# Kernel tuning notes

Measured on AMD Instinct MI355X. Metric: run time of the kernel, lower is better.

The kernel has to match this reference:

```python
import jax, jax.numpy as jnp
import numpy as np
from jax import lax

RADIUS = 0.3
NSAMPLE = 16
NPROP = 256
NHB = 12
NSC = 18
NCLS = 18
BNEPS = 1e-5


def setup_inputs() -> dict:
    key = jax.random.key(0)
    ks = jax.random.split(key, 10)
    B, K, C = 32, 2048, 256
    OUT = 2 + 3 + NHB * 2 + NSC * 4 + NCLS  # 119
    return {
        "xyz": jax.random.uniform(ks[0], (B, K, 3), jnp.float32),
        "features": jax.random.normal(ks[1], (B, C, K), jnp.float32),
        "sa_w1": jax.random.normal(ks[2], (256, C + 3), jnp.float32) * 0.05,
        "sa_w2": jax.random.normal(ks[3], (256, 256), jnp.float32) * 0.05,
        "sa_w3": jax.random.normal(ks[4], (256, 256), jnp.float32) * 0.05,
        "sa_gamma": jnp.ones((3, 256), jnp.float32),
        "sa_beta": jnp.zeros((3, 256), jnp.float32),
        "sa_mean": jnp.zeros((3, 256), jnp.float32),
        "sa_var": jnp.ones((3, 256), jnp.float32),
        "p_w1": jax.random.normal(ks[5], (256, 256), jnp.float32) * 0.05,
        "p_w2": jax.random.normal(ks[6], (256, 256), jnp.float32) * 0.05,
        "p_w3": jax.random.normal(ks[7], (OUT, 256), jnp.float32) * 0.05,
        "p_b3": jnp.zeros((OUT,), jnp.float32),
        "p_gamma": jnp.ones((2, 256), jnp.float32),
        "p_beta": jnp.zeros((2, 256), jnp.float32),
        "p_mean": jnp.zeros((2, 256), jnp.float32),
        "p_var": jnp.ones((2, 256), jnp.float32),
        "mean_size_arr": jax.random.uniform(ks[8], (NSC, 3), jnp.float32, 0.3, 1.5),
    }


def fps(xyz, npoint):
    # iterative furthest point sampling, starts at index 0 (matches CUDA kernel)
    B, K, _ = xyz.shape

    def body(carry, _):
        dist, far = carry
        centroid = jnp.take_along_axis(xyz, far[:, None, None], axis=1)  # (B,1,3)
        d = jnp.sum((xyz - centroid) ** 2, axis=-1)  # (B,K)
        dist = jnp.minimum(dist, d)
        nxt = jnp.argmax(dist, axis=-1).astype(jnp.int32)
        return (dist, nxt), far

    init = (jnp.full((B, K), 1e10, xyz.dtype), jnp.zeros((B,), jnp.int32))
    _, inds = lax.scan(body, init, None, length=npoint)
    return jnp.transpose(inds, (1, 0))  # (B, npoint)


def ball_query(new_xyz, xyz):
    # first NSAMPLE points (in original index order) within RADIUS; pad with first hit
    B, K, _ = xyz.shape
    d2 = jnp.sum((new_xyz[:, :, None, :] - xyz[:, None, :, :]) ** 2, axis=-1)  # (B,P,K)
    within = d2 < RADIUS * RADIUS
    cand = jnp.where(within, jnp.arange(K, dtype=jnp.int32)[None, None, :], K)
    cand = jnp.sort(cand, axis=-1)[..., :NSAMPLE]
    first = cand[..., :1]  # query point itself is always within radius
    return jnp.where(cand == K, first, cand)  # (B,P,NSAMPLE)


def box_corners(center_unnorm, size, angle):
    # flip_axis_to_camera: X right, Y down (-z_up), Z forward (y_up)
    cc = jnp.stack([center_unnorm[..., 0], center_unnorm[..., 2], -center_unnorm[..., 1]], axis=-1)
    c, s = jnp.cos(angle), jnp.sin(angle)
    zz, oo = jnp.zeros_like(angle), jnp.ones_like(angle)
    R = jnp.stack([c, zz, s, zz, oo, zz, -s, zz, c], axis=-1).reshape(angle.shape + (3, 3))
    sx = jnp.asarray([1, 1, -1, -1, 1, 1, -1, -1], jnp.float32)
    sy = jnp.asarray([1, 1, 1, 1, -1, -1, -1, -1], jnp.float32)
    sz = jnp.asarray([1, -1, -1, 1, 1, -1, -1, 1], jnp.float32)
    xc = size[..., 0:1] * sx * 0.5
    yc = size[..., 2:3] * sy * 0.5
    zc = size[..., 1:2] * sz * 0.5
    corners = jnp.stack([xc, yc, zc], axis=-2)  # (B,P,3,8)
    out = jnp.einsum('bpij,bpjk->bpik', R, corners) + cc[..., None]
    return jnp.transpose(out, (0, 1, 3, 2))  # (B,P,8,3)


def _forward(xyz, features, sa_w1, sa_w2, sa_w3, sa_gamma, sa_beta, sa_mean, sa_var,
             p_w1, p_w2, p_w3, p_b3, p_gamma, p_beta, p_mean, p_var, mean_size_arr):
    B, K, _ = xyz.shape
    inds = fps(xyz, NPROP)  # (B,P) vote_fps
    new_xyz = jnp.take_along_axis(xyz, inds[..., None], axis=1)  # (B,P,3)
    idx = ball_query(new_xyz, xyz)  # (B,P,S)
    flat = idx.reshape(B, -1)
    g_xyz = jnp.take_along_axis(xyz, flat[..., None], axis=1).reshape(B, NPROP, NSAMPLE, 3)
    g_xyz = (g_xyz - new_xyz[:, :, None, :]) / RADIUS  # normalize_xyz
    g_feat = jnp.take_along_axis(features, flat[:, None, :], axis=2).reshape(B, -1, NPROP, NSAMPLE)
    x = jnp.concatenate([jnp.transpose(g_xyz, (0, 3, 1, 2)), g_feat], axis=1)  # (B,3+C,P,S)
    for i, w in enumerate((sa_w1, sa_w2, sa_w3)):
        x = jnp.einsum('oc,bcps->bops', w, x)
        scale = (sa_gamma[i] / jnp.sqrt(sa_var[i] + BNEPS))[None, :, None, None]
        x = jax.nn.relu((x - sa_mean[i][None, :, None, None]) * scale + sa_beta[i][None, :, None, None])
    y = jnp.max(x, axis=-1)  # (B,256,P) max-pool over neighbors
    for i, w in enumerate((p_w1, p_w2)):
        y = jnp.einsum('oc,bcp->bop', w, y)
        scale = (p_gamma[i] / jnp.sqrt(p_var[i] + BNEPS))[None, :, None]
        y = jax.nn.relu((y - p_mean[i][None, :, None]) * scale + p_beta[i][None, :, None])
    net = jnp.einsum('oc,bcp->bop', p_w3, y) + p_b3[None, :, None]
    nt = jnp.transpose(net, (0, 2, 1))  # (B,P,119)
    obj = nt[..., 0:2]
    center = new_xyz + nt[..., 2:5]
    o = 5 + NHB * 2
    size_scores = nt[..., o:o + NSC]
    srn = nt[..., o + NSC:o + NSC * 4].reshape(B, NPROP, NSC, 3)
    sem = nt[..., o + NSC * 4:]
    size_res = srn * mean_size_arr[None, None]
    best = jnp.argmax(size_scores, axis=-1)
    pred_size = jnp.take_along_axis(size_res + mean_size_arr[None, None],
                                    best[..., None, None], axis=2)[:, :, 0, :]
    corners = box_corners(center, pred_size, jnp.zeros_like(center[..., 0]))
    sem_logits = jnp.concatenate(
        [sem, jnp.argmin(obj, axis=-1, keepdims=True).astype(nt.dtype) * 1e10], axis=-1)
    obj_prob = jax.nn.softmax(obj, axis=-1)[..., 1]
    sem_prob = jax.nn.softmax(sem, axis=-1)
    return obj, center, size_scores, size_res, pred_size, sem, corners, sem_logits, obj_prob, sem_prob


def reference(xyz, features, sa_w1, sa_w2, sa_w3, sa_gamma, sa_beta, sa_mean, sa_var,
              p_w1, p_w2, p_w3, p_b3, p_gamma, p_beta, p_mean, p_var, mean_size_arr):
    return _forward(xyz, features, sa_w1, sa_w2, sa_w3, sa_gamma, sa_beta, sa_mean, sa_var,
                    p_w1, p_w2, p_w3, p_b3, p_gamma, p_beta, p_mean, p_var, mean_size_arr)
```

## Files before the change

### kernel.cpp

```cpp
#include <hip/hip_runtime.h>
#include <math.h>

#define B_   32
#define K_   2048
#define C_   256
#define P_   256
#define S_   16
#define OUTC 119

#define OFF0 0
#define OFF1 16384
#define OFF2 40960
#define OFF3 188416
#define OFF4 630784
#define OFF5 655360
#define OFF6 802816
#define OFF7 999424
#define OFF8 1155072
#define OFF9 1163264

typedef _Float16 half8  __attribute__((ext_vector_type(8)));
typedef _Float16 half4h __attribute__((ext_vector_type(4)));
typedef float    f32x4  __attribute__((ext_vector_type(4)));
#define MFMA16 __builtin_amdgcn_mfma_f32_16x16x32_f16

__device__ __forceinline__ float sqdist_rn(float ax, float ay, float az,
                                           float bx, float by, float bz) {
  float dx = __fsub_rn(ax, bx), dy = __fsub_rn(ay, by), dz = __fsub_rn(az, bz);
  return __fadd_rn(__fadd_rn(__fmul_rn(dx, dx), __fmul_rn(dy, dy)),
                   __fmul_rn(dz, dz));
}

__device__ __forceinline__ unsigned umax_(unsigned a, unsigned b) {
  return a > b ? a : b;
}
__device__ __forceinline__ unsigned umin_(unsigned a, unsigned b) {
  return a < b ? a : b;
}
__device__ __forceinline__ unsigned wave_red_umax(unsigned x) {
  x = umax_(x, (unsigned)__builtin_amdgcn_update_dpp(0, (int)x, 0x111, 0xf, 0xf, false));
  x = umax_(x, (unsigned)__builtin_amdgcn_update_dpp(0, (int)x, 0x112, 0xf, 0xf, false));
  x = umax_(x, (unsigned)__builtin_amdgcn_update_dpp(0, (int)x, 0x114, 0xf, 0xf, false));
  x = umax_(x, (unsigned)__builtin_amdgcn_update_dpp(0, (int)x, 0x118, 0xf, 0xf, false));
  x = umax_(x, (unsigned)__builtin_amdgcn_update_dpp(0, (int)x, 0x142, 0xf, 0xf, false));
  x = umax_(x, (unsigned)__builtin_amdgcn_update_dpp(0, (int)x, 0x143, 0xf, 0xf, false));
  return x;
}
__device__ __forceinline__ unsigned wave_red_umin(unsigned x) {
  x = umin_(x, (unsigned)__builtin_amdgcn_update_dpp(-1, (int)x, 0x111, 0xf, 0xf, false));
  x = umin_(x, (unsigned)__builtin_amdgcn_update_dpp(-1, (int)x, 0x112, 0xf, 0xf, false));
  x = umin_(x, (unsigned)__builtin_amdgcn_update_dpp(-1, (int)x, 0x114, 0xf, 0xf, false));
  x = umin_(x, (unsigned)__builtin_amdgcn_update_dpp(-1, (int)x, 0x118, 0xf, 0xf, false));
  x = umin_(x, (unsigned)__builtin_amdgcn_update_dpp(-1, (int)x, 0x142, 0xf, 0xf, false));
  x = umin_(x, (unsigned)__builtin_amdgcn_update_dpp(-1, (int)x, 0x143, 0xf, 0xf, false));
  return x;
}

__device__ __forceinline__ void wsplit_body(
    int r, int t, const float* __restrict__ w1, const float* __restrict__ w2,
    const float* __restrict__ w3, const float* __restrict__ pw1,
    const float* __restrict__ pw2, const float* __restrict__ gma,
    const float* __restrict__ var, const float* __restrict__ pg,
    const float* __restrict__ pv, _Float16* __restrict__ w1h,
    _Float16* __restrict__ w1l, _Float16* __restrict__ w2h,
    _Float16* __restrict__ w2l, _Float16* __restrict__ w3h,
    _Float16* __restrict__ w3l, _Float16* __restrict__ p1h,
    _Float16* __restrict__ p1l, _Float16* __restrict__ p2h,
    _Float16* __restrict__ p2l, float* __restrict__ bns) {
  if (r == 656) {
    for (int u = t; u < 768; u += 64) bns[u] = gma[u] / sqrtf(var[u] + 1e-5f);
    for (int u = t; u < 512; u += 64)
      bns[768 + u] = pg[u] / sqrtf(pv[u] + 1e-5f);
    return;
  }
  const float* src;
  _Float16 *dh, *dl;
  int ot, ks, nks, K, remap = 0;
  if (r < 144) {
    src = w1; dh = w1h; dl = w1l; ot = r / 9; ks = r % 9; nks = 9; K = 259;
    remap = 1;
  } else if (r < 272) {
    const int rr = r - 144;
    src = w2; dh = w2h; dl = w2l; ot = rr >> 3; ks = rr & 7; nks = 8; K = 256;
  } else if (r < 400) {
    const int rr = r - 272;
    src = w3; dh = w3h; dl = w3l; ot = rr >> 3; ks = rr & 7; nks = 8; K = 256;
  } else if (r < 528) {
    const int rr = r - 400;
    src = pw1; dh = p1h; dl = p1l; ot = rr >> 3; ks = rr & 7; nks = 8; K = 256;
  } else {
    const int rr = r - 528;
    src = pw2; dh = p2h; dl = p2l; ot = rr >> 3; ks = rr & 7; nks = 8; K = 256;
  }
  const int m = t & 15, q = t >> 4;
  const float* row = src + (ot * 16 + m) * K;
  half8 vh, vl;
#pragma unroll
  for (int j = 0; j < 8; j++) {
    const int c = ks * 32 + q * 8 + j;
    float v;
    if (remap) {
      v = (c < 3) ? row[c] : (c >= 8 && c < 264) ? row[c - 5] : 0.f;
    } else {
      v = (c < K) ? row[c] : 0.f;
    }
    const _Float16 hi = (_Float16)v;
    vh[j] = hi;
    vl[j] = (_Float16)(v - (float)hi);
  }
  const int base = ((ot * nks + ks) * 64 + t) * 8;
  *(half8*)&dh[base] = vh;
  *(half8*)&dl[base] = vl;
}

__global__ __launch_bounds__(256) void fused_pre_kernel(
    const float* __restrict__ xyz, float* __restrict__ new_xyz,
    const float* __restrict__ features, _Float16* __restrict__ ftH,
    _Float16* __restrict__ ftL,
    const float* __restrict__ w1, const float* __restrict__ w2,
    const float* __restrict__ w3, const float* __restrict__ pw1,
    const float* __restrict__ pw2, const float* __restrict__ gma,
    const float* __restrict__ var, const float* __restrict__ pg,
    const float* __restrict__ pv, _Float16* __restrict__ w1h,
    _Float16* __restrict__ w1l, _Float16* __restrict__ w2h,
    _Float16* __restrict__ w2l, _Float16* __restrict__ w3h,
    _Float16* __restrict__ w3l, _Float16* __restrict__ p1h,
    _Float16* __restrict__ p1l, _Float16* __restrict__ p2h,
    _Float16* __restrict__ p2l, float* __restrict__ bns) {
  __shared__ __align__(16) char smem_pre[32768];
  __shared__ uint2 redw[2][4];
  const int bid = blockIdx.x;

  if (bid >= 197) {
    const int idx = bid - 197;
    const int b = idx >> 7, rem = idx & 127;
    const int c0 = (rem >> 5) * 64, k0 = (rem & 31) * 64;
    float* tl = (float*)smem_pre;
    const int w = threadIdx.x >> 6, lane = threadIdx.x & 63;
    const float* fb = features + (size_t)b * C_ * K_;
#pragma unroll
    for (int r = 0; r < 16; r++) {
      const int cl = r * 4 + w;
      tl[cl * 65 + lane] = fb[(size_t)(c0 + cl) * K_ + k0 + lane];
    }
    __syncthreads();
#pragma unroll
    for (int r = 0; r < 16; r++) {
      const int kl = r * 4 + w;
      const float v = tl[lane * 65 + kl];
      const _Float16 hi = (_Float16)v;
      const size_t o = ((size_t)b * K_ + k0 + kl) * C_ + c0 + lane;
      ftH[o] = hi;
      ftL[o] = (_Float16)(v - (float)hi);
    }
    return;
  }

  if (bid >= 32) {
    const int sub = (bid - 32) * 4 + (threadIdx.x >> 6);
    if (sub < 657)
      wsplit_body(sub, threadIdx.x & 63, w1, w2, w3, pw1, pw2, gma, var, pg,
                  pv, w1h, w1l, w2h, w2l, w3h, w3l, p1h, p1l, p2h, p2l, bns);
    return;
  }

  const int b = bid, t = threadIdx.x;
  const int lane = t & 63, w = t >> 6;
  float4* pts = (float4*)smem_pre;
  const float* xb = xyz + b * K_ * 3;
  float px[8], py[8], pz[8], dist[8];
#pragma unroll
  for (int j = 0; j < 8; j++) {
    const int k = t + 256 * j;
    const float x = xb[3 * k + 0];
    const float yv = xb[3 * k + 1];
    const float z = xb[3 * k + 2];
    px[j] = x; py[j] = yv; pz[j] = z;
    dist[j] = 1e10f;
    pts[k] = make_float4(x, yv, z, 0.f);
  }
  __syncthreads();
  int far = 0;
  for (int i = 0; i < P_; i++) {
    const float4 c = pts[far];
    if (t == 0) {
      float* nx = new_xyz + (b * P_ + i) * 3;
      nx[0] = c.x; nx[1] = c.y; nx[2] = c.z;
    }
    float bv = -1.f;
    int bj = 0;
#pragma unroll
    for (int j = 0; j < 8; j++) {
      const float d = sqdist_rn(px[j], py[j], pz[j], c.x, c.y, c.z);
      dist[j] = fminf(dist[j], d);
      if (dist[j] > bv) { bv = dist[j]; bj = j; }
    }
    const unsigned bvb = __float_as_uint(bv);
    const unsigned gw = wave_red_umax(bvb);
    const unsigned gmaxw = (unsigned)__builtin_amdgcn_readlane((int)gw, 63);
    const unsigned kg = (unsigned)(bj * 256 + t);
    const unsigned key2 = (bvb == gmaxw) ? kg : 0xFFFFFFFFu;
    const unsigned kw = wave_red_umin(key2);
    if (lane == 63) redw[i & 1][w] = make_uint2(gmaxw, kw);
    __syncthreads();
    const uint2 r0 = redw[i & 1][0], r1 = redw[i & 1][1];
    const uint2 r2 = redw[i & 1][2], r3 = redw[i & 1][3];
    const unsigned g = umax_(umax_(r0.x, r1.x), umax_(r2.x, r3.x));
    unsigned fk = 0xFFFFFFFFu;
    if (r0.x == g) fk = umin_(fk, r0.y);
    if (r1.x == g) fk = umin_(fk, r1.y);
    if (r2.x == g) fk = umin_(fk, r2.y);
    if (r3.x == g) fk = umin_(fk, r3.y);
    far = (int)fk;
  }
}

__global__ __launch_bounds__(1024) void ballq_kernel(
    const float* __restrict__ xyz, const float* __restrict__ new_xyz,
    int* __restrict__ idxw) {
  const int blk = blockIdx.x;
  const int b = blk >> 4, pg = (blk & 15) * 16, t = threadIdx.x;
  __shared__ __align__(16) float4 pts[K_];
  const float* xb = xyz + b * K_ * 3;
#pragma unroll
  for (int j = 0; j < 2; j++) {
    const int k = t + 1024 * j;
    pts[k] = make_float4(xb[3 * k + 0], xb[3 * k + 1], xb[3 * k + 2], 0.f);
  }
  __syncthreads();
  const float r2 = (float)(0.3 * 0.3);
  const int w = t >> 6, lane = t & 63;
  const int p = pg + w;
  const float nx = new_xyz[(b * P_ + p) * 3 + 0];
  const float ny = new_xyz[(b * P_ + p) * 3 + 1];
  const float nz = new_xyz[(b * P_ + p) * 3 + 2];
  int* ob = idxw + (b * P_ + p) * S_;
  unsigned msk = 0u;
#pragma unroll
  for (int j = 0; j < 32; j++) {
    const float4 q = pts[j * 64 + lane];
    const float d2 = sqdist_rn(q.x, q.y, q.z, nx, ny, nz);
    msk |= (d2 < r2 ? 1u : 0u) << j;
  }
  int cnt = 0, first = -1;
  for (int j = 0; j < 32; j++) {
    const unsigned long long bal = __ballot((msk >> j) & 1u);
    if (bal != 0ull && first < 0) first = j * 64 + (__ffsll(bal) - 1);
    const int c = (int)__popcll(bal);
    if ((msk >> j) & 1u) {
      const int pos = cnt + (int)__popcll(bal & ((1ull << lane) - 1ull));
      if (pos < S_) ob[pos] = j * 64 + lane;
    }
    cnt += c;
    if (cnt >= S_) break;
  }
  if (cnt < S_ && lane < S_ - cnt) ob[cnt + lane] = first;
}

__global__ __launch_bounds__(512, 4) void sa_kernel(
    const float* __restrict__ xyz, const float* __restrict__ features,
    const _Float16* __restrict__ ftH, const _Float16* __restrict__ ftL,
    const int use_ft,
    const _Float16* __restrict__ w1h, const _Float16* __restrict__ w1l,
    const _Float16* __restrict__ w2h, const _Float16* __restrict__ w2l,
    const _Float16* __restrict__ w3h, const _Float16* __restrict__ w3l,
    const float* __restrict__ bns, const float* __restrict__ mu,
    const float* __restrict__ bta, const float* __restrict__ new_xyz,
    const int* __restrict__ idxw, float* __restrict__ y) {
  const int blk = blockIdx.x;
  const int b = blk >> 7, p0 = (blk & 127) * 2, t = threadIdx.x;
  __shared__ __align__(16) _Float16 X1h[18 * 64 * 8];
  __shared__ __align__(16) _Float16 X1l[18 * 64 * 8];
  __shared__ __align__(16) _Float16 X2h[16 * 64 * 8];
  __shared__ __align__(16) _Float16 X2l[16 * 64 * 8];
  __shared__ __align__(16) float red[2 * 256];
  __shared__ int k_sh[32];

  if (t < 32) k_sh[t] = idxw[(b * P_ + p0) * S_ + t];
  if (t < 96) {
    const int tile = 16 + (t / 48), rem = t % 48;
    const int row = tile * 64 + 16 + rem;
    const half8 z8 = {};
    *(half8*)&X1h[row * 8] = z8;
    *(half8*)&X1l[row * 8] = z8;
  }
  __syncthreads();
  if (t < 32) {
    const int st = t >> 4, m = t & 15, k = k_sh[t];
    const float* xb = xyz + b * K_ * 3;
    const float* nx = new_xyz + (b * P_ + p0 + st) * 3;
    const int base = (st * 64 + m) * 8;
#pragma unroll
    for (int c = 0; c < 3; c++) {
      const float v = (xb[3 * k + c] - nx[c]) / 0.3f;
      const _Float16 hi = (_Float16)v;
      X1h[base + c] = hi;
      X1l[base + c] = (_Float16)(v - (float)hi);
    }
#pragma unroll
    for (int j = 3; j < 8; j++) {
      X1h[base + j] = (_Float16)0.f;
      X1l[base + j] = (_Float16)0.f;
    }
  }
  if (use_ft) {
    for (int u = t; u < 1024; u += 512) {
      const int s = u >> 5, ch = u & 31;
      const int c = 8 + ch * 8;
      const int ks = c >> 5, q2 = (c >> 3) & 3;
      const int st = s >> 4, m = s & 15;
      const size_t ro = ((size_t)b * K_ + k_sh[s]) * C_ + ch * 8;
      const int dst = ((ks * 2 + st) * 64 + q2 * 16 + m) * 8;
      *(half8*)&X1h[dst] = *(const half8*)&ftH[ro];
      *(half8*)&X1l[dst] = *(const half8*)&ftL[ro];
    }
  } else {
    const int cl = t & 255, hf = t >> 8;
    const float* fb = features + (size_t)b * C_ * K_ + (size_t)cl * K_;
    const int c = 8 + cl;
    const int ks = c >> 5, q2 = (c >> 3) & 3, j = c & 7;
    const int s0 = hf * 16;
#pragma unroll 8
    for (int s = s0; s < s0 + 16; s++) {
      const float v = fb[k_sh[s]];
      const _Float16 hi = (_Float16)v;
      const int dst = ((ks * 2 + (s >> 4)) * 64 + q2 * 16 + (s & 15)) * 8 + j;
      X1h[dst] = hi;
      X1l[dst] = (_Float16)(v - (float)hi);
    }
  }

  const int lane = t & 63, w = t >> 6;
  const int m = lane & 15, q = lane >> 4;

  f32x4 acc[2][2];
  half8 rAh[2][2], rAl[2][2];
#pragma unroll
  for (int i = 0; i < 2; i++) {
    rAh[0][i] = *(const half8*)&w1h[(((2 * w + i) * 9 + 0) * 64 + lane) * 8];
    rAl[0][i] = *(const half8*)&w1l[(((2 * w + i) * 9 + 0) * 64 + lane) * 8];
    rAh[1][i] = *(const half8*)&w1h[(((2 * w + i) * 9 + 1) * 64 + lane) * 8];
    rAl[1][i] = *(const half8*)&w1l[(((2 * w + i) * 9 + 1) * 64 + lane) * 8];
  }
  __syncthreads();

#pragma unroll
  for (int l = 0; l < 3; l++) {
    const _Float16* Xih = (l == 1) ? X2h : X1h;
    const _Float16* Xil = (l == 1) ? X2l : X1l;
    const int nks = (l == 0) ? 9 : 8;
    const int base = (l == 0) ? 0 : (l == 1) ? 9 : 17;
#pragma unroll
    for (int i = 0; i < 2; i++) {
      acc[i][0] = (f32x4){0.f, 0.f, 0.f, 0.f};
      acc[i][1] = (f32x4){0.f, 0.f, 0.f, 0.f};
    }
#pragma unroll
    for (int ks = 0; ks < nks; ks++) {
      const int par = (base + ks) & 1;
      half8 Ah[2], Al[2];
#pragma unroll
      for (int i = 0; i < 2; i++) { Ah[i] = rAh[par][i]; Al[i] = rAl[par][i]; }
      {
        int ln = l, kn = ks + 2;
        if (kn >= nks) { kn -= nks; ln = l + 1; }
        if (ln < 3) {
          const _Float16* Ph = (ln == 0) ? w1h : (ln == 1) ? w2h : w3h;
          const _Float16* Pl = (ln == 0) ? w1l : (ln == 1) ? w2l : w3l;
          const int nk2 = (ln == 0) ? 9 : 8;
#pragma unroll
          for (int i = 0; i < 2; i++) {
            const int off = (((2 * w + i) * nk2 + kn) * 64 + lane) * 8;
            rAh[par][i] = *(const half8*)&Ph[off];
            rAl[par][i] = *(const half8*)&Pl[off];
          }
        }
      }
      const int tb = (ks * 2) * 512 + lane * 8;
      const half8 Bh0 = *(const half8*)&Xih[tb];
      const half8 Bl0 = *(const half8*)&Xil[tb];
      const half8 Bh1 = *(const half8*)&Xih[tb + 512];
      const half8 Bl1 = *(const half8*)&Xil[tb + 512];
#pragma unroll
      for (int i = 0; i < 2; i++) {
        acc[i][0] = MFMA16(Ah[i], Bh0, acc[i][0], 0, 0, 0);
        acc[i][0] = MFMA16(Ah[i], Bl0, acc[i][0], 0, 0, 0);
        acc[i][0] = MFMA16(Al[i], Bh0, acc[i][0], 0, 0, 0);
        acc[i][1] = MFMA16(Ah[i], Bh1, acc[i][1], 0, 0, 0);
        acc[i][1] = MFMA16(Ah[i], Bl1, acc[i][1], 0, 0, 0);
        acc[i][1] = MFMA16(Al[i], Bh1, acc[i][1], 0, 0, 0);
      }
    }

    if (l < 2) {
      _Float16* Xoh = (l == 0) ? X2h : X1h;
      _Float16* Xol = (l == 0) ? X2l : X1l;
#pragma unroll
      for (int i = 0; i < 2; i++) {
        const int c0 = (2 * w + i) * 16 + q * 4;
        const int ks2 = c0 >> 5, q2 = (c0 >> 3) & 3, j0 = c0 & 7;
        const f32x4 sc4 = *(const f32x4*)&bns[l * 256 + c0];
        const f32x4 m4 = *(const f32x4*)&mu[l * 256 + c0];
        const f32x4 b4 = *(const f32x4*)&bta[l * 256 + c0];
#pragma unroll
        for (int s = 0; s < 2; s++) {
          half4h vh, vl;
#pragma unroll
          for (int r = 0; r < 4; r++) {
            const float v = fmaxf((acc[i][s][r] - m4[r]) * sc4[r] + b4[r], 0.f);
            const _Float16 hi = (_Float16)v;
            vh[r] = hi;
            vl[r] = (_Float16)(v - (float)hi);
          }
          const int dst = ((ks2 * 2 + s) * 64 + q2 * 16 + m) * 8 + j0;
          *(half4h*)&Xoh[dst] = vh;
          *(half4h*)&Xol[dst] = vl;
        }
      }
      __syncthreads();
    } else {
#pragma unroll
      for (int i = 0; i < 2; i++)
#pragma unroll
        for (int s = 0; s < 2; s++)
#pragma unroll
          for (int r = 0; r < 4; r++) {
            float v = acc[i][s][r];
            v = fmaxf(v, __shfl_xor(v, 1));
            v = fmaxf(v, __shfl_xor(v, 2));
            v = fmaxf(v, __shfl_xor(v, 4));
            v = fmaxf(v, __shfl_xor(v, 8));
            acc[i][s][r] = v;
          }
      if (m == 0) {
#pragma unroll
        for (int i = 0; i < 2; i++) {
          const int ob = (2 * w + i) * 16 + q * 4;
          *(f32x4*)&red[ob] = acc[i][0];
          *(f32x4*)&red[256 + ob] = acc[i][1];
        }
      }
      __syncthreads();
      const int pl = t >> 8, col = t & 255;
      const float sc2 = bns[512 + col];
      const float mu2 = mu[512 + col], bt2 = bta[512 + col];
      const float raw = red[pl * 256 + col];
      y[(b * P_ + p0 + pl) * 256 + col] = fmaxf((raw - mu2) * sc2 + bt2, 0.f);
    }
  }
}

__global__ __launch_bounds__(256, 2) void phead_kernel(
    const float* __restrict__ y, const _Float16* __restrict__ p1h,
    const _Float16* __restrict__ p1l, const _Float16* __restrict__ p2h,
    const _Float16* __restrict__ p2l, const float* __restrict__ pw3,
    const float* __restrict__ pb3, const float* __restrict__ bns,
    const float* __restrict__ pm, const float* __restrict__ pb,
    const float* __restrict__ new_xyz, const float* __restrict__ msa,
    float* __restrict__ out) {
  const int blk = blockIdx.x;
  const int b = blk >> 4, p0 = (blk & 15) * 16, t = threadIdx.x;
  __shared__ __align__(16) char smem[58624];
  _Float16* X0h = (_Float16*)smem;
  _Float16* X0l = (_Float16*)(smem + 8448);
  _Float16* Hh  = (_Float16*)(smem + 16896);
  _Float16* Hl  = (_Float16*)(smem + 25344);
  float*    Wt  = (float*)smem;
  float*    Y2  = (float*)(smem + 33792);
  float*    net_s = (float*)(smem + 50432);

  {
#pragma unroll 4
    for (int s = 0; s < 16; s++) {
      const float v = y[(size_t)(b * P_ + p0 + s) * C_ + t];
      const _Float16 hi = (_Float16)v;
      X0h[s * 264 + t] = hi;
      X0l[s * 264 + t] = (_Float16)(v - (float)hi);
    }
  }
  const int lane = t & 63, w = t >> 6;
  const int m = lane & 15, q = lane >> 4;

  f32x4 acc[4];
  half8 pAh[4], pAl[4];
#pragma unroll
  for (int i = 0; i < 4; i++) {
    const int off = (((4 * w + i) * 8) * 64 + lane) * 8;
    pAh[i] = *(const half8*)&p1h[off];
    pAl[i] = *(const half8*)&p1l[off];
  }
  __syncthreads();

#pragma unroll
  for (int l = 0; l < 2; l++) {
    const _Float16* Xih = l ? Hh : X0h;
    const _Float16* Xil = l ? Hl : X0l;
#pragma unroll
    for (int i = 0; i < 4; i++) acc[i] = (f32x4){0.f, 0.f, 0.f, 0.f};
    for (int ks = 0; ks < 8; ks++) {
      half8 Ah[4], Al[4];
#pragma unroll
      for (int i = 0; i < 4; i++) { Ah[i] = pAh[i]; Al[i] = pAl[i]; }
      {
        int ln = l, kn = ks + 1;
        if (kn == 8) { ln = l + 1; kn = 0; }
        if (ln < 2) {
          const _Float16* Ph = ln ? p2h : p1h;
          const _Float16* Pl = ln ? p2l : p1l;
#pragma unroll
          for (int i = 0; i < 4; i++) {
            const int off = (((4 * w + i) * 8 + kn) * 64 + lane) * 8;
            pAh[i] = *(const half8*)&Ph[off];
            pAl[i] = *(const half8*)&Pl[off];
          }
        }
      }
      const int xo = ks * 32 + q * 8;
      const half8 Bh = *(const half8*)&Xih[m * 264 + xo];
      const half8 Bl = *(const half8*)&Xil[m * 264 + xo];
#pragma unroll
      for (int i = 0; i < 4; i++) {
        acc[i] = MFMA16(Ah[i], Bh, acc[i], 0, 0, 0);
        acc[i] = MFMA16(Ah[i], Bl, acc[i], 0, 0, 0);
        acc[i] = MFMA16(Al[i], Bh, acc[i], 0, 0, 0);
      }
    }
#pragma unroll
    for (int i = 0; i < 4; i++) {
      const int ob = (4 * w + i) * 16 + q * 4;
      const f32x4 sc4 = *(const f32x4*)&bns[768 + l * 256 + ob];
      const f32x4 m4 = *(const f32x4*)&pm[l * 256 + ob];
      const f32x4 b4 = *(const f32x4*)&pb[l * 256 + ob];
      if (l == 0) {
        half4h vh, vl;
#pragma unroll
        for (int r = 0; r < 4; r++) {
          const float v = fmaxf((acc[i][r] - m4[r]) * sc4[r] + b4[r], 0.f);
          const _Float16 hi = (_Float16)v;
          vh[r] = hi;
          vl[r] = (_Float16)(v - (float)hi);
        }
        *(half4h*)&Hh[m * 264 + ob] = vh;
        *(half4h*)&Hl[m * 264 + ob] = vl;
      } else {
        f32x4 r4;
#pragma unroll
        for (int r = 0; r < 4; r++)
          r4[r] = fmaxf((acc[i][r] - m4[r]) * sc4[r] + b4[r], 0.f);
        *(f32x4*)&Y2[m * 260 + ob] = r4;
      }
    }
    __syncthreads();
  }

  {
    const int o = t & 127, ph = t >> 7;
    float a3[8];
#pragma unroll
    for (int pp = 0; pp < 8; pp++) a3[pp] = 0.f;
    for (int tile = 0; tile < 16; tile++) {
      const int c0 = tile * 16;
      for (int u = t; u < 119 * 4; u += 256) {
        int oo = u >> 2, qq = u & 3;
        *(float4*)&Wt[(qq * 128 + oo) * 4] =
            *(const float4*)(pw3 + oo * 256 + c0 + qq * 4);
      }
      __syncthreads();
      if (o < 119) {
#pragma unroll
        for (int j4 = 0; j4 < 4; j4++) {
          const float4 wv = *(const float4*)&Wt[(j4 * 128 + o) * 4];
#pragma unroll
          for (int pp = 0; pp < 8; pp++) {
            const float4 xv =
                *(const float4*)&Y2[(ph * 8 + pp) * 260 + c0 + j4 * 4];
            a3[pp] = fmaf(wv.x, xv.x, a3[pp]);
            a3[pp] = fmaf(wv.y, xv.y, a3[pp]);
            a3[pp] = fmaf(wv.z, xv.z, a3[pp]);
            a3[pp] = fmaf(wv.w, xv.w, a3[pp]);
          }
        }
      }
      __syncthreads();
    }
    if (o < 119) {
      const float bb = pb3[o];
#pragma unroll
      for (int pp = 0; pp < 8; pp++)
        net_s[(ph * 8 + pp) * 120 + o] = a3[pp] + bb;
    }
  }
  __syncthreads();

  if (t < 16) {
    const int gi = b * P_ + p0 + t;
    const float* nr = &net_s[t * 120];
    const float nx = new_xyz[gi * 3 + 0];
    const float ny = new_xyz[gi * 3 + 1];
    const float nz = new_xyz[gi * 3 + 2];
    const float obj0 = nr[0], obj1 = nr[1];
    out[OFF0 + gi * 2 + 0] = obj0;
    out[OFF0 + gi * 2 + 1] = obj1;
    const float cx = nx + nr[2], cy = ny + nr[3], cz = nz + nr[4];
    out[OFF1 + gi * 3 + 0] = cx;
    out[OFF1 + gi * 3 + 1] = cy;
    out[OFF1 + gi * 3 + 2] = cz;
    float bv = -1e30f;
    int bi = 0;
#pragma unroll
    for (int i = 0; i < 18; i++) {
      float v = nr[29 + i];
      out[OFF2 + gi * 18 + i] = v;
      if (v > bv) { bv = v; bi = i; }
    }
#pragma unroll
    for (int i = 0; i < 18; i++)
#pragma unroll
      for (int j = 0; j < 3; j++)
        out[OFF3 + gi * 54 + i * 3 + j] =
            __fmul_rn(nr[47 + i * 3 + j], msa[i * 3 + j]);
    float ps[3];
#pragma unroll
    for (int j = 0; j < 3; j++) {
      ps[j] = __fadd_rn(__fmul_rn(nr[47 + bi * 3 + j], msa[bi * 3 + j]),
                        msa[bi * 3 + j]);
      out[OFF4 + gi * 3 + j] = ps[j];
    }
    float sm = -1e30f;
#pragma unroll
    for (int i = 0; i < 18; i++) {
      float v = nr[101 + i];
      out[OFF5 + gi * 18 + i] = v;
      out[OFF7 + gi * 19 + i] = v;
      sm = fmaxf(sm, v);
    }
    out[OFF7 + gi * 19 + 18] = (obj0 <= obj1) ? 0.f : 1e10f;
    const float cc0 = cx, cc1 = cz, cc2 = -cy;
    const float sxk[8] = {1, 1, -1, -1, 1, 1, -1, -1};
    const float syk[8] = {1, 1, 1, 1, -1, -1, -1, -1};
    const float szk[8] = {1, -1, -1, 1, 1, -1, -1, 1};
#pragma unroll
    for (int k = 0; k < 8; k++) {
      out[OFF6 + gi * 24 + 3 * k + 0] = cc0 + ps[0] * sxk[k] * 0.5f;
      out[OFF6 + gi * 24 + 3 * k + 1] = cc1 + ps[2] * syk[k] * 0.5f;
      out[OFF6 + gi * 24 + 3 * k + 2] = cc2 + ps[1] * szk[k] * 0.5f;
    }
    {
      const float m2 = fmaxf(obj0, obj1);
      const float e0 = expf(obj0 - m2), e1 = expf(obj1 - m2);
      out[OFF8 + gi] = e1 / (e0 + e1);
    }
    {
      float ev[18], es = 0.f;
#pragma unroll
      for (int i = 0; i < 18; i++) {
        ev[i] = expf(nr[101 + i] - sm);
        es += ev[i];
      }
#pragma unroll
      for (int i = 0; i < 18; i++) out[OFF9 + gi * 18 + i] = ev[i] / es;
    }
  }
}

extern "C" void kernel_launch(void* const* d_in, const int* in_sizes, int n_in,
                              void* d_out, int out_size, void* d_ws,
                              size_t ws_size, hipStream_t stream) {
  (void)in_sizes; (void)n_in; (void)out_size;
  const float* xyz      = (const float*)d_in[0];
  const float* features = (const float*)d_in[1];
  const float* w1       = (const float*)d_in[2];
  const float* w2       = (const float*)d_in[3];
  const float* w3       = (const float*)d_in[4];
  const float* gma      = (const float*)d_in[5];
  const float* bta      = (const float*)d_in[6];
  const float* mu       = (const float*)d_in[7];
  const float* var      = (const float*)d_in[8];
  const float* pw1      = (const float*)d_in[9];
  const float* pw2      = (const float*)d_in[10];
  const float* pw3      = (const float*)d_in[11];
  const float* pb3      = (const float*)d_in[12];
  const float* pg       = (const float*)d_in[13];
  const float* pb       = (const float*)d_in[14];
  const float* pm       = (const float*)d_in[15];
  const float* pv       = (const float*)d_in[16];
  const float* msa      = (const float*)d_in[17];
  float* out = (float*)d_out;

  char* ws = (char*)d_ws;
  float*     new_xyz = (float*)ws;
  int*       idxw    = (int*)(ws + 98304);
  float*     yb      = (float*)(ws + 622592);
  _Float16*  w1h     = (_Float16*)(ws + 9011200);
  _Float16*  w1l     = (_Float16*)(ws + 9158656);
  _Float16*  w2h     = (_Float16*)(ws + 9306112);
  _Float16*  w2l     = (_Float16*)(ws + 9437184);
  _Float16*  w3h     = (_Float16*)(ws + 9568256);
  _Float16*  w3l     = (_Float16*)(ws + 9699328);
  float*     bns     = (float*)(ws + 9830400);
  _Float16*  p1h     = (_Float16*)(ws + 9835520);
  _Float16*  p1l     = (_Float16*)(ws + 9966592);
  _Float16*  p2h     = (_Float16*)(ws + 10097664);
  _Float16*  p2l     = (_Float16*)(ws + 10228736);
  _Float16*  ftH     = (_Float16*)(ws + 10359808);
  _Float16*  ftL     = (_Float16*)(ws + 43914240);

  const int use_ft = (ws_size >= 77468672ull) ? 1 : 0;
  const int npre = use_ft ? (197 + 4096) : 197;

  fused_pre_kernel<<<npre, 256, 0, stream>>>(xyz, new_xyz, features, ftH, ftL,
                                             w1, w2, w3, pw1, pw2, gma, var,
                                             pg, pv, w1h, w1l, w2h, w2l, w3h,
                                             w3l, p1h, p1l, p2h, p2l, bns);
  ballq_kernel<<<B_ * 16, 1024, 0, stream>>>(xyz, new_xyz, idxw);
  sa_kernel<<<B_ * 128, 512, 0, stream>>>(xyz, features, ftH, ftL, use_ft,
                                          w1h, w1l, w2h, w2l, w3h, w3l, bns,
                                          mu, bta, new_xyz, idxw, yb);
  phead_kernel<<<B_ * 16, 256, 0, stream>>>(yb, p1h, p1l, p2h, p2l, pw3, pb3,
                                            bns, pm, pb, new_xyz, msa, out);
}
```

Measured before the change: 449.3 us.

## Process four proposals per SA block with single swizzled in-place LDS buffer

```diff
diff --git a/kernel.cpp b/kernel.cpp
--- a/kernel.cpp
+++ b/kernel.cpp
@@ -23,6 +23,8 @@
 typedef _Float16 half4h __attribute__((ext_vector_type(4)));
 typedef float    f32x4  __attribute__((ext_vector_type(4)));
 #define MFMA16 __builtin_amdgcn_mfma_f32_16x16x32_f16
+
+#define XT 65
 
 __device__ __forceinline__ float sqdist_rn(float ax, float ay, float az,
                                            float bx, float by, float bz) {
@@ -268,72 +270,71 @@
     const float* __restrict__ bta, const float* __restrict__ new_xyz,
     const int* __restrict__ idxw, float* __restrict__ y) {
   const int blk = blockIdx.x;
-  const int b = blk >> 7, p0 = (blk & 127) * 2, t = threadIdx.x;
-  __shared__ __align__(16) _Float16 X1h[18 * 64 * 8];
-  __shared__ __align__(16) _Float16 X1l[18 * 64 * 8];
-  __shared__ __align__(16) _Float16 X2h[16 * 64 * 8];
-  __shared__ __align__(16) _Float16 X2l[16 * 64 * 8];
-  __shared__ __align__(16) float red[2 * 256];
-  __shared__ int k_sh[32];
-
-  if (t < 32) k_sh[t] = idxw[(b * P_ + p0) * S_ + t];
-  if (t < 96) {
-    const int tile = 16 + (t / 48), rem = t % 48;
-    const int row = tile * 64 + 16 + rem;
+  const int b = blk >> 6, p0 = (blk & 63) * 4, t = threadIdx.x;
+  __shared__ __align__(16) _Float16 Xh[36 * XT * 8];
+  __shared__ __align__(16) _Float16 Xl[36 * XT * 8];
+  __shared__ __align__(16) float red[4 * 256];
+  __shared__ int k_sh[64];
+
+  if (t < 64) k_sh[t] = idxw[(b * P_ + p0) * S_ + t];
+  if (t < 192) {
+    const int tile = 32 + t / 48, row = 16 + (t % 48);
     const half8 z8 = {};
-    *(half8*)&X1h[row * 8] = z8;
-    *(half8*)&X1l[row * 8] = z8;
+    *(half8*)&Xh[(tile * XT + row) * 8] = z8;
+    *(half8*)&Xl[(tile * XT + row) * 8] = z8;
   }
   __syncthreads();
-  if (t < 32) {
+  if (t < 64) {
     const int st = t >> 4, m = t & 15, k = k_sh[t];
     const float* xb = xyz + b * K_ * 3;
     const float* nx = new_xyz + (b * P_ + p0 + st) * 3;
-    const int base = (st * 64 + m) * 8;
+    const int base = (st * XT + m) * 8;
 #pragma unroll
     for (int c = 0; c < 3; c++) {
       const float v = (xb[3 * k + c] - nx[c]) / 0.3f;
       const _Float16 hi = (_Float16)v;
-      X1h[base + c] = hi;
-      X1l[base + c] = (_Float16)(v - (float)hi);
+      Xh[base + c] = hi;
+      Xl[base + c] = (_Float16)(v - (float)hi);
     }
 #pragma unroll
     for (int j = 3; j < 8; j++) {
-      X1h[base + j] = (_Float16)0.f;
-      X1l[base + j] = (_Float16)0.f;
+      Xh[base + j] = (_Float16)0.f;
+      Xl[base + j] = (_Float16)0.f;
     }
   }
   if (use_ft) {
-    for (int u = t; u < 1024; u += 512) {
+    for (int u = t; u < 2048; u += 512) {
       const int s = u >> 5, ch = u & 31;
       const int c = 8 + ch * 8;
       const int ks = c >> 5, q2 = (c >> 3) & 3;
       const int st = s >> 4, m = s & 15;
       const size_t ro = ((size_t)b * K_ + k_sh[s]) * C_ + ch * 8;
-      const int dst = ((ks * 2 + st) * 64 + q2 * 16 + m) * 8;
-      *(half8*)&X1h[dst] = *(const half8*)&ftH[ro];
-      *(half8*)&X1l[dst] = *(const half8*)&ftL[ro];
+      const int row = (q2 * 16 + m) ^ (ks & 7);
+      const int dst = ((ks * 4 + st) * XT + row) * 8;
+      *(half8*)&Xh[dst] = *(const half8*)&ftH[ro];
+      *(half8*)&Xl[dst] = *(const half8*)&ftL[ro];
     }
   } else {
     const int cl = t & 255, hf = t >> 8;
     const float* fb = features + (size_t)b * C_ * K_ + (size_t)cl * K_;
     const int c = 8 + cl;
     const int ks = c >> 5, q2 = (c >> 3) & 3, j = c & 7;
-    const int s0 = hf * 16;
+    const int s0 = hf * 32;
 #pragma unroll 8
-    for (int s = s0; s < s0 + 16; s++) {
+    for (int s = s0; s < s0 + 32; s++) {
       const float v = fb[k_sh[s]];
       const _Float16 hi = (_Float16)v;
-      const int dst = ((ks * 2 + (s >> 4)) * 64 + q2 * 16 + (s & 15)) * 8 + j;
-      X1h[dst] = hi;
-      X1l[dst] = (_Float16)(v - (float)hi);
+      const int row = (q2 * 16 + (s & 15)) ^ (ks & 7);
+      const int dst = ((ks * 4 + (s >> 4)) * XT + row) * 8 + j;
+      Xh[dst] = hi;
+      Xl[dst] = (_Float16)(v - (float)hi);
     }
   }
 
   const int lane = t & 63, w = t >> 6;
   const int m = lane & 15, q = lane >> 4;
 
-  f32x4 acc[2][2];
+  f32x4 acc[2][4];
   half8 rAh[2][2], rAl[2][2];
 #pragma unroll
   for (int i = 0; i < 2; i++) {
@@ -346,15 +347,12 @@
 
 #pragma unroll
   for (int l = 0; l < 3; l++) {
-    const _Float16* Xih = (l == 1) ? X2h : X1h;
-    const _Float16* Xil = (l == 1) ? X2l : X1l;
     const int nks = (l == 0) ? 9 : 8;
     const int base = (l == 0) ? 0 : (l == 1) ? 9 : 17;
 #pragma unroll
-    for (int i = 0; i < 2; i++) {
-      acc[i][0] = (f32x4){0.f, 0.f, 0.f, 0.f};
-      acc[i][1] = (f32x4){0.f, 0.f, 0.f, 0.f};
-    }
+    for (int i = 0; i < 2; i++)
+#pragma unroll
+      for (int s = 0; s < 4; s++) acc[i][s] = (f32x4){0.f, 0.f, 0.f, 0.f};
 #pragma unroll
     for (int ks = 0; ks < nks; ks++) {
       const int par = (base + ks) & 1;
@@ -376,25 +374,23 @@
           }
         }
       }
-      const int tb = (ks * 2) * 512 + lane * 8;
-      const half8 Bh0 = *(const half8*)&Xih[tb];
-      const half8 Bl0 = *(const half8*)&Xil[tb];
-      const half8 Bh1 = *(const half8*)&Xih[tb + 512];
-      const half8 Bl1 = *(const half8*)&Xil[tb + 512];
-#pragma unroll
-      for (int i = 0; i < 2; i++) {
-        acc[i][0] = MFMA16(Ah[i], Bh0, acc[i][0], 0, 0, 0);
-        acc[i][0] = MFMA16(Ah[i], Bl0, acc[i][0], 0, 0, 0);
-        acc[i][0] = MFMA16(Al[i], Bh0, acc[i][0], 0, 0, 0);
-        acc[i][1] = MFMA16(Ah[i], Bh1, acc[i][1], 0, 0, 0);
-        acc[i][1] = MFMA16(Ah[i], Bl1, acc[i][1], 0, 0, 0);
-        acc[i][1] = MFMA16(Al[i], Bh1, acc[i][1], 0, 0, 0);
+      const int rsw = lane ^ (ks & 7);
+#pragma unroll
+      for (int s = 0; s < 4; s++) {
+        const int tb = ((ks * 4 + s) * XT + rsw) * 8;
+        const half8 Bh = *(const half8*)&Xh[tb];
+        const half8 Bl = *(const half8*)&Xl[tb];
+#pragma unroll
+        for (int i = 0; i < 2; i++) {
+          acc[i][s] = MFMA16(Ah[i], Bh, acc[i][s], 0, 0, 0);
+          acc[i][s] = MFMA16(Ah[i], Bl, acc[i][s], 0, 0, 0);
+          acc[i][s] = MFMA16(Al[i], Bh, acc[i][s], 0, 0, 0);
+        }
       }
     }
 
     if (l < 2) {
-      _Float16* Xoh = (l == 0) ? X2h : X1h;
-      _Float16* Xol = (l == 0) ? X2l : X1l;
+      __syncthreads();
 #pragma unroll
       for (int i = 0; i < 2; i++) {
         const int c0 = (2 * w + i) * 16 + q * 4;
@@ -402,8 +398,9 @@
         const f32x4 sc4 = *(const f32x4*)&bns[l * 256 + c0];
         const f32x4 m4 = *(const f32x4*)&mu[l * 256 + c0];
         const f32x4 b4 = *(const f32x4*)&bta[l * 256 + c0];
-#pragma unroll
-        for (int s = 0; s < 2; s++) {
+        const int row = (q2 * 16 + m) ^ (ks2 & 7);
+#pragma unroll
+        for (int s = 0; s < 4; s++) {
           half4h vh, vl;
 #pragma unroll
           for (int r = 0; r < 4; r++) {
@@ -412,9 +409,9 @@
             vh[r] = hi;
             vl[r] = (_Float16)(v - (float)hi);
           }
-          const int dst = ((ks2 * 2 + s) * 64 + q2 * 16 + m) * 8 + j0;
-          *(half4h*)&Xoh[dst] = vh;
-          *(half4h*)&Xol[dst] = vl;
+          const int dst = ((ks2 * 4 + s) * XT + row) * 8 + j0;
+          *(half4h*)&Xh[dst] = vh;
+          *(half4h*)&Xl[dst] = vl;
         }
       }
       __syncthreads();
@@ -422,7 +419,7 @@
 #pragma unroll
       for (int i = 0; i < 2; i++)
 #pragma unroll
-        for (int s = 0; s < 2; s++)
+        for (int s = 0; s < 4; s++)
 #pragma unroll
           for (int r = 0; r < 4; r++) {
             float v = acc[i][s][r];
@@ -436,16 +433,18 @@
 #pragma unroll
         for (int i = 0; i < 2; i++) {
           const int ob = (2 * w + i) * 16 + q * 4;
-          *(f32x4*)&red[ob] = acc[i][0];
-          *(f32x4*)&red[256 + ob] = acc[i][1];
+#pragma unroll
+          for (int s = 0; s < 4; s++) *(f32x4*)&red[s * 256 + ob] = acc[i][s];
         }
       }
       __syncthreads();
-      const int pl = t >> 8, col = t & 255;
-      const float sc2 = bns[512 + col];
-      const float mu2 = mu[512 + col], bt2 = bta[512 + col];
-      const float raw = red[pl * 256 + col];
-      y[(b * P_ + p0 + pl) * 256 + col] = fmaxf((raw - mu2) * sc2 + bt2, 0.f);
+      for (int u = t; u < 1024; u += 512) {
+        const int pl = u >> 8, col = u & 255;
+        const float sc2 = bns[512 + col];
+        const float mu2 = mu[512 + col], bt2 = bta[512 + col];
+        const float raw = red[pl * 256 + col];
+        y[(b * P_ + p0 + pl) * 256 + col] = fmaxf((raw - mu2) * sc2 + bt2, 0.f);
+      }
     }
   }
 }
@@ -713,9 +712,9 @@
                                              pg, pv, w1h, w1l, w2h, w2l, w3h,
                                              w3l, p1h, p1l, p2h, p2l, bns);
   ballq_kernel<<<B_ * 16, 1024, 0, stream>>>(xyz, new_xyz, idxw);
-  sa_kernel<<<B_ * 128, 512, 0, stream>>>(xyz, features, ftH, ftL, use_ft,
-                                          w1h, w1l, w2h, w2l, w3h, w3l, bns,
-                                          mu, bta, new_xyz, idxw, yb);
+  sa_kernel<<<B_ * 64, 512, 0, stream>>>(xyz, features, ftH, ftL, use_ft,
+                                         w1h, w1l, w2h, w2l, w3h, w3l, bns,
+                                         mu, bta, new_xyz, idxw, yb);
   phead_kernel<<<B_ * 16, 256, 0, stream>>>(yb, p1h, p1l, p2h, p2l, pw3, pb3,
                                             bns, pm, pb, new_xyz, msa, out);
 }
```

Measured after the change: 432.1 us. 3.8% less time.
